# Kernel optimization log

Measured on AMD Instinct MI355X. Metric: run time of the kernel, lower is better.

Reference implementation:

```python
import jax, jax.numpy as jnp
import numpy as np

NOISE_STD = 0.1
TOP_K = 2


def setup_inputs() -> dict:
    key = jax.random.key(0)
    k_x, k_n, k_w, k_keys = jax.random.split(key, 4)
    N, D_IN, D_Q, K = 16384, 2048, 256, 64
    x = jax.random.normal(k_x, (N, D_IN), dtype=jnp.float32)
    noise = jax.random.normal(k_n, (N, K), dtype=jnp.float32)
    # Linear params (kaiming-uniform-ish scale) and xavier-uniform keys
    w_q = jax.random.normal(k_w, (D_IN, D_Q), dtype=jnp.float32) * (1.0 / np.sqrt(D_IN))
    b_q = jnp.zeros((D_Q,), dtype=jnp.float32)
    lim = np.sqrt(6.0 / (K + D_Q))
    keys = jax.random.uniform(k_keys, (K, D_Q), dtype=jnp.float32, minval=-lim, maxval=lim)
    return {"x": x, "noise": noise, "w_q": w_q, "b_q": b_q, "keys": keys}


def reference(x, noise, w_q, b_q, keys):
    # query projection: [N, D_in] @ [D_in, D_q] -> [N, D_q]
    query = x @ w_q + b_q
    d_q = query.shape[-1]
    # router logits: [N, K], scaled dot product with expert keys
    logits = (query @ keys.T) * (1.0 / jnp.sqrt(jnp.asarray(d_q, query.dtype)))
    logits = logits + noise * NOISE_STD  # training-mode gating noise
    # top-k selection + softmax over selected logits only
    top_logits, top_idx = jax.lax.top_k(logits, TOP_K)       # [N, top_k]
    top_probs = jax.nn.softmax(top_logits, axis=-1)           # [N, top_k]
    # scatter selected probs into dense [N, K] gating tensor (zeros elsewhere)
    rows = jnp.arange(logits.shape[0])[:, None]               # [N, 1]
    gating_probs = jnp.zeros_like(logits).at[rows, top_idx].set(top_probs)
    return gating_probs, top_idx
```

## Files before the change

kernel.cpp:

```cpp
#include <hip/hip_runtime.h>

#define MROWS 16384
#define KD 2048
#define NQ 256
#define NE 64
#define INV_SQRT_DQ 0.0625f
#define NOISE_STD_C 0.1f

typedef _Float16 f16x8 __attribute__((ext_vector_type(8)));
typedef float f32x4 __attribute__((ext_vector_type(4)));

__device__ inline void split8v(f32x4 a, f32x4 b, f16x8* h, f16x8* l) {
    f16x8 hh, ll;
#pragma unroll
    for (int i = 0; i < 4; ++i) {
        _Float16 s = (_Float16)a[i];
        hh[i] = s; ll[i] = (_Float16)(a[i] - (float)s);
    }
#pragma unroll
    for (int i = 0; i < 4; ++i) {
        _Float16 s = (_Float16)b[i];
        hh[4 + i] = s; ll[4 + i] = (_Float16)(b[i] - (float)s);
    }
    *h = hh; *l = ll;
}

__global__ void prep_w(const float* __restrict__ w, _Float16* __restrict__ whp,
                       _Float16* __restrict__ wlp) {
    const int tid = blockIdx.x * 256 + threadIdx.x;
    const int f    = tid & 15;
    const int q    = (tid >> 4) & 3;
    const int ngrp = (tid >> 6) & 15;
    const int kcs  = tid >> 10;
    const int n = ngrp * 16 + f;
    const int k = kcs * 32 + q * 8;
    f16x8 h, l;
#pragma unroll
    for (int j = 0; j < 8; ++j) {
        float v = w[(size_t)(k + j) * NQ + n];
        _Float16 s = (_Float16)v;
        h[j] = s;
        l[j] = (_Float16)(v - (float)s);
    }
    *(f16x8*)(whp + (size_t)tid * 8) = h;
    *(f16x8*)(wlp + (size_t)tid * 8) = l;
}

__global__ __launch_bounds__(512) void gemm_fused(
    const float* __restrict__ x, const _Float16* __restrict__ whp,
    const _Float16* __restrict__ wlp, const float* __restrict__ bq,
    const float* __restrict__ keys, const float* __restrict__ noise,
    float* __restrict__ gate, float* __restrict__ idxout) {
    __shared__ __align__(16) char smem[66560];

    const int t = threadIdx.x;
    const int lane = t & 63;
    const int wv = t >> 6;
    const int m0 = blockIdx.x * 64;
    const int f = lane & 15;
    const int qq = lane >> 4;
    const int aswz = (f & 7) * 8;

    const int srow = t >> 3;
    const int sk8 = (t & 7) * 8;
    const int scol = sk8 ^ ((srow & 7) * 8);
    const f32x4* xp = (const f32x4*)(x + (size_t)(m0 + srow) * KD + sk8);

    const _Float16* bph = whp + (size_t)(2 * wv) * 512 + lane * 8;
    const _Float16* bpl = wlp + (size_t)(2 * wv) * 512 + lane * 8;

    f32x4 acc[4][2];
#pragma unroll
    for (int mt = 0; mt < 4; ++mt)
#pragma unroll
        for (int nt = 0; nt < 2; ++nt) acc[mt][nt] = {0.f, 0.f, 0.f, 0.f};

    f16x8 bhC[2][2], blC[2][2], bhN[2][2], blN[2][2];

    f32x4 xa = __builtin_nontemporal_load(xp);
    f32x4 xb = __builtin_nontemporal_load(xp + 1);
#pragma unroll
    for (int ks = 0; ks < 2; ++ks)
#pragma unroll
        for (int nt = 0; nt < 2; ++nt) {
            size_t o = (size_t)ks * 8192 + nt * 512;
            bhC[ks][nt] = *(const f16x8*)(bph + o);
            blC[ks][nt] = *(const f16x8*)(bpl + o);
        }
    {
        f16x8 h8, l8;
        split8v(xa, xb, &h8, &l8);
        *(f16x8*)((_Float16*)smem + srow * 64 + scol) = h8;
        *(f16x8*)((_Float16*)(smem + 8192) + srow * 64 + scol) = l8;
    }
    xa = __builtin_nontemporal_load(xp + 16);
    xb = __builtin_nontemporal_load(xp + 17);
    __syncthreads();

    for (int i = 0; i < 32; ++i) {
        const int cb = i & 1;
        _Float16* AhC = (_Float16*)(smem + cb * 16384);
        _Float16* AlC = AhC + 4096;
        _Float16* AhN = (_Float16*)(smem + (cb ^ 1) * 16384);
        _Float16* AlN = AhN + 4096;

        if (i + 1 < 32) {
            size_t base = (size_t)(2 * (i + 1)) * 8192;
#pragma unroll
            for (int ks = 0; ks < 2; ++ks)
#pragma unroll
                for (int nt = 0; nt < 2; ++nt) {
                    size_t o = base + (size_t)ks * 8192 + nt * 512;
                    bhN[ks][nt] = *(const f16x8*)(bph + o);
                    blN[ks][nt] = *(const f16x8*)(bpl + o);
                }
        }
        if (i + 1 < 32) {
            f16x8 h8, l8;
            split8v(xa, xb, &h8, &l8);
            *(f16x8*)(AhN + srow * 64 + scol) = h8;
            *(f16x8*)(AlN + srow * 64 + scol) = l8;
        }
        if (i + 2 < 32) {
            xa = __builtin_nontemporal_load(xp + (i + 2) * 16);
            xb = __builtin_nontemporal_load(xp + (i + 2) * 16 + 1);
        }
#pragma unroll
        for (int ks = 0; ks < 2; ++ks) {
            f16x8 ah[4], al[4];
#pragma unroll
            for (int mt = 0; mt < 4; ++mt) {
                int ab = (mt * 16 + f) * 64 + ((ks * 32 + qq * 8) ^ aswz);
                ah[mt] = *(const f16x8*)(AhC + ab);
                al[mt] = *(const f16x8*)(AlC + ab);
            }
#pragma unroll
            for (int mt = 0; mt < 4; ++mt)
#pragma unroll
                for (int nt = 0; nt < 2; ++nt) {
                    acc[mt][nt] = __builtin_amdgcn_mfma_f32_16x16x32_f16(ah[mt], bhC[ks][nt], acc[mt][nt], 0, 0, 0);
                    acc[mt][nt] = __builtin_amdgcn_mfma_f32_16x16x32_f16(ah[mt], blC[ks][nt], acc[mt][nt], 0, 0, 0);
                    acc[mt][nt] = __builtin_amdgcn_mfma_f32_16x16x32_f16(al[mt], bhC[ks][nt], acc[mt][nt], 0, 0, 0);
                }
        }
#pragma unroll
        for (int ks = 0; ks < 2; ++ks)
#pragma unroll
            for (int nt = 0; nt < 2; ++nt) {
                bhC[ks][nt] = bhN[ks][nt];
                blC[ks][nt] = blN[ks][nt];
            }
        asm volatile("" ::: "memory");
        __builtin_amdgcn_s_waitcnt(0xC07F);
        __builtin_amdgcn_s_barrier();
        asm volatile("" ::: "memory");
    }

    float* qs = (float*)smem;
#pragma unroll
    for (int nt = 0; nt < 2; ++nt) {
        int col = wv * 32 + nt * 16 + f;
        float bias = bq[col];
#pragma unroll
        for (int mt = 0; mt < 4; ++mt)
#pragma unroll
            for (int r = 0; r < 4; ++r)
                qs[(mt * 16 + qq * 4 + r) * 260 + col] = acc[mt][nt][r] + bias;
    }
    __syncthreads();

    const int e = wv * 16 + f;
    f32x4 a2[4];
#pragma unroll
    for (int mt = 0; mt < 4; ++mt) a2[mt] = {0.f, 0.f, 0.f, 0.f};
    if (wv < 4) {
        const float* kp = keys + (size_t)e * NQ + qq * 8;
        for (int kc = 0; kc < NQ; kc += 32) {
            f32x4 b0 = *(const f32x4*)(kp + kc);
            f32x4 b1 = *(const f32x4*)(kp + kc + 4);
            f16x8 bh2, bl2;
            split8v(b0, b1, &bh2, &bl2);
#pragma unroll
            for (int mt = 0; mt < 4; ++mt) {
                const float* ap = qs + (mt * 16 + f) * 260 + kc + qq * 8;
                f32x4 a0 = *(const f32x4*)ap;
                f32x4 a1 = *(const f32x4*)(ap + 4);
                f16x8 ah2, al2;
                split8v(a0, a1, &ah2, &al2);
                a2[mt] = __builtin_amdgcn_mfma_f32_16x16x32_f16(ah2, bh2, a2[mt], 0, 0, 0);
                a2[mt] = __builtin_amdgcn_mfma_f32_16x16x32_f16(ah2, bl2, a2[mt], 0, 0, 0);
                a2[mt] = __builtin_amdgcn_mfma_f32_16x16x32_f16(al2, bh2, a2[mt], 0, 0, 0);
            }
        }
    }
    __syncthreads();

    float* LG = (float*)smem;
    if (wv < 4) {
#pragma unroll
        for (int mt = 0; mt < 4; ++mt)
#pragma unroll
            for (int r = 0; r < 4; ++r) {
                int row = mt * 16 + qq * 4 + r;
                LG[row * 65 + e] = a2[mt][r] * INV_SQRT_DQ +
                                   NOISE_STD_C * noise[(size_t)(m0 + row) * NE + e];
            }
    }
    __syncthreads();

    for (int i = 0; i < 8; ++i) {
        int r = wv * 8 + i;
        float v = LG[r * 65 + lane];
        float v1 = v; int i1 = lane;
#pragma unroll
        for (int off = 32; off; off >>= 1) {
            float ov = __shfl_xor(v1, off);
            int oi = __shfl_xor(i1, off);
            if (ov > v1 || (ov == v1 && oi < i1)) { v1 = ov; i1 = oi; }
        }
        float v2 = (lane == i1) ? -1e30f : v;
        int i2 = lane;
#pragma unroll
        for (int off = 32; off; off >>= 1) {
            float ov = __shfl_xor(v2, off);
            int oi = __shfl_xor(i2, off);
            if (ov > v2 || (ov == v2 && oi < i2)) { v2 = ov; i2 = oi; }
        }
        float ex = expf(v2 - v1);
        float p1 = 1.0f / (1.0f + ex);
        float p2 = ex * p1;
        float g = (lane == i1) ? p1 : ((lane == i2) ? p2 : 0.0f);
        gate[(size_t)(m0 + r) * NE + lane] = g;
        if (lane == 0) {
            float2 ii = make_float2((float)i1, (float)i2);
            *(float2*)(idxout + (size_t)(m0 + r) * 2) = ii;
        }
    }
}

extern "C" void kernel_launch(void* const* d_in, const int* in_sizes, int n_in,
                              void* d_out, int out_size, void* d_ws, size_t ws_size,
                              hipStream_t stream) {
    const float* x     = (const float*)d_in[0];
    const float* noise = (const float*)d_in[1];
    const float* w_q   = (const float*)d_in[2];
    const float* b_q   = (const float*)d_in[3];
    const float* keys  = (const float*)d_in[4];
    float* out = (float*)d_out;

    char* ws = (char*)d_ws;
    _Float16* whp = (_Float16*)ws;
    _Float16* wlp = (_Float16*)(ws + (1u << 20));

    prep_w<<<256, 256, 0, stream>>>(w_q, whp, wlp);
    gemm_fused<<<256, 512, 0, stream>>>(x, whp, wlp, b_q, keys, noise,
                                        out, out + (size_t)MROWS * NE);
}
```

Baseline: 229.7 us.

## Double K-tile per barrier and stream B fragments per k-substep with MFMA priority

The main GEMM loop now stages a 128-wide K slab of x (64 rows, split into fp16 hi/lo) per iteration, halving the number of iterations and barriers from 32 to 16. Weight fragments are prefetched one k-substep ahead in a two-slot rotating register buffer instead of a whole iteration ahead. MFMA blocks are wrapped in s_setprio to favour the matrix issue. The aim is to cut barrier and sync overhead and reduce register pressure from B prefetch, at the cost of more LDS per stage and a shorter prefetch distance for B.

```diff
diff --git a/kernel.cpp b/kernel.cpp
--- a/kernel.cpp
+++ b/kernel.cpp
@@ -59,12 +59,12 @@
     const int m0 = blockIdx.x * 64;
     const int f = lane & 15;
     const int qq = lane >> 4;
-    const int aswz = (f & 7) * 8;
-
-    const int srow = t >> 3;
-    const int sk8 = (t & 7) * 8;
-    const int scol = sk8 ^ ((srow & 7) * 8);
-    const f32x4* xp = (const f32x4*)(x + (size_t)(m0 + srow) * KD + sk8);
+
+    const int srow = t >> 4;
+    const int soct = t & 15;
+    const int swoff = (soct ^ (srow & 7)) * 8;
+    const f32x4* xq0 = (const f32x4*)(x + (size_t)(m0 + srow) * KD + soct * 8);
+    const f32x4* xq1 = (const f32x4*)(x + (size_t)(m0 + srow + 32) * KD + soct * 8);
 
     const _Float16* bph = whp + (size_t)(2 * wv) * 512 + lane * 8;
     const _Float16* bpl = wlp + (size_t)(2 * wv) * 512 + lane * 8;
@@ -75,81 +75,85 @@
 #pragma unroll
         for (int nt = 0; nt < 2; ++nt) acc[mt][nt] = {0.f, 0.f, 0.f, 0.f};
 
-    f16x8 bhC[2][2], blC[2][2], bhN[2][2], blN[2][2];
-
-    f32x4 xa = __builtin_nontemporal_load(xp);
-    f32x4 xb = __builtin_nontemporal_load(xp + 1);
-#pragma unroll
-    for (int ks = 0; ks < 2; ++ks)
-#pragma unroll
-        for (int nt = 0; nt < 2; ++nt) {
-            size_t o = (size_t)ks * 8192 + nt * 512;
-            bhC[ks][nt] = *(const f16x8*)(bph + o);
-            blC[ks][nt] = *(const f16x8*)(bpl + o);
-        }
+    f32x4 a0 = __builtin_nontemporal_load(xq0);
+    f32x4 a1 = __builtin_nontemporal_load(xq0 + 1);
+    f32x4 b0 = __builtin_nontemporal_load(xq1);
+    f32x4 b1 = __builtin_nontemporal_load(xq1 + 1);
     {
+        _Float16* Ah = (_Float16*)smem;
+        _Float16* Al = Ah + 8192;
         f16x8 h8, l8;
-        split8v(xa, xb, &h8, &l8);
-        *(f16x8*)((_Float16*)smem + srow * 64 + scol) = h8;
-        *(f16x8*)((_Float16*)(smem + 8192) + srow * 64 + scol) = l8;
-    }
-    xa = __builtin_nontemporal_load(xp + 16);
-    xb = __builtin_nontemporal_load(xp + 17);
-    __syncthreads();
-
-    for (int i = 0; i < 32; ++i) {
-        const int cb = i & 1;
-        _Float16* AhC = (_Float16*)(smem + cb * 16384);
-        _Float16* AlC = AhC + 4096;
-        _Float16* AhN = (_Float16*)(smem + (cb ^ 1) * 16384);
-        _Float16* AlN = AhN + 4096;
-
-        if (i + 1 < 32) {
-            size_t base = (size_t)(2 * (i + 1)) * 8192;
-#pragma unroll
-            for (int ks = 0; ks < 2; ++ks)
-#pragma unroll
-                for (int nt = 0; nt < 2; ++nt) {
-                    size_t o = base + (size_t)ks * 8192 + nt * 512;
-                    bhN[ks][nt] = *(const f16x8*)(bph + o);
-                    blN[ks][nt] = *(const f16x8*)(bpl + o);
-                }
-        }
-        if (i + 1 < 32) {
+        split8v(a0, a1, &h8, &l8);
+        *(f16x8*)(Ah + srow * 128 + swoff) = h8;
+        *(f16x8*)(Al + srow * 128 + swoff) = l8;
+        split8v(b0, b1, &h8, &l8);
+        *(f16x8*)(Ah + (srow + 32) * 128 + swoff) = h8;
+        *(f16x8*)(Al + (srow + 32) * 128 + swoff) = l8;
+    }
+    a0 = __builtin_nontemporal_load(xq0 + 32);
+    a1 = __builtin_nontemporal_load(xq0 + 33);
+    b0 = __builtin_nontemporal_load(xq1 + 32);
+    b1 = __builtin_nontemporal_load(xq1 + 33);
+    __syncthreads();
+
+    f16x8 bh[2][2], bl[2][2];
+#pragma unroll
+    for (int nt = 0; nt < 2; ++nt) {
+        bh[0][nt] = *(const f16x8*)(bph + nt * 512);
+        bl[0][nt] = *(const f16x8*)(bpl + nt * 512);
+    }
+
+    for (int i = 0; i < 16; ++i) {
+        _Float16* AhC = (_Float16*)smem + (i & 1) * 16384;
+        _Float16* AlC = AhC + 8192;
+        _Float16* AhN = (_Float16*)smem + ((i & 1) ^ 1) * 16384;
+        _Float16* AlN = AhN + 8192;
+
+        if (i < 15) {
             f16x8 h8, l8;
-            split8v(xa, xb, &h8, &l8);
-            *(f16x8*)(AhN + srow * 64 + scol) = h8;
-            *(f16x8*)(AlN + srow * 64 + scol) = l8;
-        }
-        if (i + 2 < 32) {
-            xa = __builtin_nontemporal_load(xp + (i + 2) * 16);
-            xb = __builtin_nontemporal_load(xp + (i + 2) * 16 + 1);
-        }
-#pragma unroll
-        for (int ks = 0; ks < 2; ++ks) {
+            split8v(a0, a1, &h8, &l8);
+            *(f16x8*)(AhN + srow * 128 + swoff) = h8;
+            *(f16x8*)(AlN + srow * 128 + swoff) = l8;
+            split8v(b0, b1, &h8, &l8);
+            *(f16x8*)(AhN + (srow + 32) * 128 + swoff) = h8;
+            *(f16x8*)(AlN + (srow + 32) * 128 + swoff) = l8;
+        }
+        if (i < 14) {
+            a0 = __builtin_nontemporal_load(xq0 + (i + 2) * 32);
+            a1 = __builtin_nontemporal_load(xq0 + (i + 2) * 32 + 1);
+            b0 = __builtin_nontemporal_load(xq1 + (i + 2) * 32);
+            b1 = __builtin_nontemporal_load(xq1 + (i + 2) * 32 + 1);
+        }
+#pragma unroll
+        for (int ks = 0; ks < 4; ++ks) {
+            const int cs = ks & 1;
+            const int ns = cs ^ 1;
+            int kcn = i * 4 + ks + 1;
+            if (kcn > 63) kcn = 63;
+            const size_t bo = (size_t)kcn * 8192;
+#pragma unroll
+            for (int nt = 0; nt < 2; ++nt) {
+                bh[ns][nt] = *(const f16x8*)(bph + bo + nt * 512);
+                bl[ns][nt] = *(const f16x8*)(bpl + bo + nt * 512);
+            }
             f16x8 ah[4], al[4];
 #pragma unroll
             for (int mt = 0; mt < 4; ++mt) {
-                int ab = (mt * 16 + f) * 64 + ((ks * 32 + qq * 8) ^ aswz);
+                const int ab = (mt * 16 + f) * 128 + (((ks * 4 + qq) ^ (f & 7)) * 8);
                 ah[mt] = *(const f16x8*)(AhC + ab);
                 al[mt] = *(const f16x8*)(AlC + ab);
             }
+            __builtin_amdgcn_s_setprio(1);
 #pragma unroll
             for (int mt = 0; mt < 4; ++mt)
 #pragma unroll
                 for (int nt = 0; nt < 2; ++nt) {
-                    acc[mt][nt] = __builtin_amdgcn_mfma_f32_16x16x32_f16(ah[mt], bhC[ks][nt], acc[mt][nt], 0, 0, 0);
-                    acc[mt][nt] = __builtin_amdgcn_mfma_f32_16x16x32_f16(ah[mt], blC[ks][nt], acc[mt][nt], 0, 0, 0);
-                    acc[mt][nt] = __builtin_amdgcn_mfma_f32_16x16x32_f16(al[mt], bhC[ks][nt], acc[mt][nt], 0, 0, 0);
+                    acc[mt][nt] = __builtin_amdgcn_mfma_f32_16x16x32_f16(ah[mt], bh[cs][nt], acc[mt][nt], 0, 0, 0);
+                    acc[mt][nt] = __builtin_amdgcn_mfma_f32_16x16x32_f16(ah[mt], bl[cs][nt], acc[mt][nt], 0, 0, 0);
+                    acc[mt][nt] = __builtin_amdgcn_mfma_f32_16x16x32_f16(al[mt], bh[cs][nt], acc[mt][nt], 0, 0, 0);
                 }
-        }
-#pragma unroll
-        for (int ks = 0; ks < 2; ++ks)
-#pragma unroll
-            for (int nt = 0; nt < 2; ++nt) {
-                bhC[ks][nt] = bhN[ks][nt];
-                blC[ks][nt] = blN[ks][nt];
-            }
+            __builtin_amdgcn_s_setprio(0);
+        }
         asm volatile("" ::: "memory");
         __builtin_amdgcn_s_waitcnt(0xC07F);
         __builtin_amdgcn_s_barrier();
@@ -176,17 +180,17 @@
     if (wv < 4) {
         const float* kp = keys + (size_t)e * NQ + qq * 8;
         for (int kc = 0; kc < NQ; kc += 32) {
-            f32x4 b0 = *(const f32x4*)(kp + kc);
-            f32x4 b1 = *(const f32x4*)(kp + kc + 4);
+            f32x4 k0 = *(const f32x4*)(kp + kc);
+            f32x4 k1 = *(const f32x4*)(kp + kc + 4);
             f16x8 bh2, bl2;
-            split8v(b0, b1, &bh2, &bl2);
+            split8v(k0, k1, &bh2, &bl2);
 #pragma unroll
             for (int mt = 0; mt < 4; ++mt) {
                 const float* ap = qs + (mt * 16 + f) * 260 + kc + qq * 8;
-                f32x4 a0 = *(const f32x4*)ap;
-                f32x4 a1 = *(const f32x4*)(ap + 4);
+                f32x4 q0 = *(const f32x4*)ap;
+                f32x4 q1 = *(const f32x4*)(ap + 4);
                 f16x8 ah2, al2;
-                split8v(a0, a1, &ah2, &al2);
+                split8v(q0, q1, &ah2, &al2);
                 a2[mt] = __builtin_amdgcn_mfma_f32_16x16x32_f16(ah2, bh2, a2[mt], 0, 0, 0);
                 a2[mt] = __builtin_amdgcn_mfma_f32_16x16x32_f16(ah2, bl2, a2[mt], 0, 0, 0);
                 a2[mt] = __builtin_amdgcn_mfma_f32_16x16x32_f16(al2, bh2, a2[mt], 0, 0, 0);
```

After: 233.3 us. About the same (+1.6%).
